# Kernel optimization log

Hardware: AMD Instinct MI355X
Metric: run time of the kernel (lower is better)

Reference implementation:

```python
import jax, jax.numpy as jnp
import numpy as np

B, L, D, K_F = 2, 1024, 768, 16  # batch, seq_len, n_embd, num_eigh**2
N_FFT = 2048


def setup_inputs() -> dict:
    key = jax.random.key(0)
    k1, k2, k3, k4 = jax.random.split(key, 4)
    x = jax.random.normal(k1, (B, L, D), dtype=jnp.float32)
    phi = jax.random.normal(k2, (L, K_F), dtype=jnp.float32) * 0.1
    M_phi_plus = jax.random.normal(k3, (K_F, D, D), dtype=jnp.float32) * (1.0 / np.sqrt(K_F * D))
    M_phi_minus = jax.random.normal(k4, (K_F, D, D), dtype=jnp.float32) * (1.0 / np.sqrt(K_F * D))
    return {"x": x, "phi": phi, "M_phi_plus": M_phi_plus, "M_phi_minus": M_phi_minus, "n": N_FFT}


def _convolve(u, v, n):
    """FFT causal convolution with K spectral filters (flash-stu `convolve`, use_approx=False).
    u: [B, L, D] inputs; v: [L, K] filters; n: FFT length (>= 2L-1 padded pow2).
    Returns U_plus, U_minus: [B, L, K, D].
    """
    b, l, d = u.shape
    sgn = jnp.where(jnp.arange(l) % 2 == 0, 1.0, -1.0).astype(u.dtype)  # alternating +/-
    # Stack the plain and sign-modulated signals: [B, L, 1, D, 2]
    U = jnp.stack([u, u * sgn[None, :, None]], axis=-1)[:, :, None, :, :]
    Uf = jnp.fft.rfft(U, n=n, axis=1)                      # [B, F, 1, D, 2] complex
    vf = jnp.fft.rfft(v, n=n, axis=0)[None, :, :, None, None]  # [1, F, K, 1, 1]
    conv = jnp.fft.irfft(vf * Uf, n=n, axis=1)[:, :l]      # [B, L, K, D, 2]
    U_plus = conv[..., 0]
    U_minus = conv[..., 1] * sgn[None, :, None, None]
    return U_plus, U_minus


def reference(x, phi, M_phi_plus, M_phi_minus, n):
    U_plus, U_minus = _convolve(x, phi, n)
    # tensordot(U, M, dims=([2,3],[0,2])): contract eigenmode k and input channel i
    spectral_plus = jnp.einsum('blki,koi->blo', U_plus, M_phi_plus)
    spectral_minus = jnp.einsum('blki,koi->blo', U_minus, M_phi_minus)
    return spectral_plus + spectral_minus
```

## Files before the change

kernel.cpp:

```cpp
#include <hip/hip_runtime.h>
#include <hip/hip_fp16.h>

typedef unsigned short u16;
typedef unsigned int   u32;
typedef _Float16 f16;
typedef __attribute__((ext_vector_type(8))) f16 f16x8;
typedef __attribute__((ext_vector_type(2))) __fp16 fp16x2;
typedef __attribute__((ext_vector_type(4))) float f32x4;

#define B_SZ  2
#define L_SEQ 1024
#define D_EMB 768
#define KF    16
#define MDIM  (B_SZ * L_SEQ)
#define KROW  (KF * D_EMB)
#define MELEM ((size_t)KF * D_EMB * D_EMB)
#define NTILE 96
#define PT_SZ 16384

__device__ __forceinline__ void gload16(const void* g, void* l) {
    __builtin_amdgcn_global_load_lds(
        (const __attribute__((address_space(1))) u32*)g,
        (__attribute__((address_space(3))) u32*)l, 16, 0, 0);
}

__global__ __launch_bounds__(256) void stu_setup(const float* __restrict__ x,
                                                 const float* __restrict__ phi,
                                                 u16* __restrict__ xT,
                                                 u16* __restrict__ Ttab) {
    __shared__ __align__(16) float xs[64][68];
    const int bid = blockIdx.x;
    const int tid = threadIdx.x;

    if (bid < 384) {
        const int s0 = (bid & 15) << 6;
        const int d0 = ((bid >> 4) % 12) << 6;
        const int b  = bid / 192;

#pragma unroll
        for (int j = 0; j < 4; ++j) {
            int c = tid + (j << 8);
            int row = c >> 4;
            int col = (c & 15) << 2;
            *(float4*)&xs[row][col] =
                *(const float4*)&x[((size_t)b * L_SEQ + s0 + row) * D_EMB + d0 + col];
        }
        __syncthreads();

        const int dl = tid >> 2;
        const int ss = (tid & 3) << 4;
        const int dg = d0 + dl;
        const int xorv = (dg & 7) << 3;

        union { u16 v[16]; uint4 q[2]; } pk;
#pragma unroll
        for (int u = 0; u < 16; ++u)
            pk.v[u] = __half_as_ushort(__float2half(xs[ss + u][dl]));

        size_t base = (size_t)b * D_EMB * L_SEQ + (size_t)dg * L_SEQ + s0;
        *(uint4*)&xT[base + ( ss      ^ xorv)] = pk.q[0];
        *(uint4*)&xT[base + ((ss + 8) ^ xorv)] = pk.q[1];
    } else {
        const int f    = bid - 384;
        const int q    = f & 15;
        const int k    = (f >> 4) & 15;
        const int sign = f >> 8;
        const int tt   = tid >> 2;
        const int ss0  = (tid & 3) << 4;

        union { u16 v[16]; uint4 q4[2]; } pk;
#pragma unroll
        for (int u = 0; u < 16; ++u) {
            int s = (q << 6) + tt - (ss0 + u);
            float v = (s >= 0 && s < L_SEQ) ? phi[s * KF + k] : 0.f;
            if (sign && (s & 1)) v = -v;
            pk.v[u] = __half_as_ushort(__float2half(v));
        }
        const int xorv = (tt & 7) << 3;
        u16* tile = Ttab + (((size_t)(sign * KF + k) * 16 + q) << 12);
        *(uint4*)&tile[(tt << 6) + ( ss0      ^ xorv)] = pk.q4[0];
        *(uint4*)&tile[(tt << 6) + ((ss0 + 8) ^ xorv)] = pk.q4[1];
    }
}

__global__ __launch_bounds__(256) void stu_conv_mcvt(
        const u16* __restrict__ xT, const u16* __restrict__ Ttab,
        u16* __restrict__ Up, u16* __restrict__ Um,
        const float* __restrict__ Mp, const float* __restrict__ Mm,
        u16* __restrict__ Hp, u16* __restrict__ Hm) {
    __shared__ __align__(16) u16 Xs[2][192 * 64];
    __shared__ __align__(16) u16 Tps[2][64 * 64];
    __shared__ __align__(16) u16 Tms[2][64 * 64];

    const int bid = blockIdx.x;
    const int tid = threadIdx.x;

    if (bid < 512) {
        const size_t n8 = MELEM / 8;
        size_t i = (size_t)bid * 256 + tid;
        const size_t stride = (size_t)512 * 256;
        for (size_t cc = i; cc < n8; cc += stride) {
            const size_t g = cc << 3;
            {
                const float4 a0 = *(const float4*)&Mp[g];
                const float4 a1 = *(const float4*)&Mp[g + 4];
                union { fp16x2 h2[4]; uint4 q; } u;
                u.h2[0] = __builtin_amdgcn_cvt_pkrtz(a0.x, a0.y);
                u.h2[1] = __builtin_amdgcn_cvt_pkrtz(a0.z, a0.w);
                u.h2[2] = __builtin_amdgcn_cvt_pkrtz(a1.x, a1.y);
                u.h2[3] = __builtin_amdgcn_cvt_pkrtz(a1.z, a1.w);
                *(uint4*)&Hp[g] = u.q;
            }
            {
                const float4 a0 = *(const float4*)&Mm[g];
                const float4 a1 = *(const float4*)&Mm[g + 4];
                union { fp16x2 h2[4]; uint4 q; } u;
                u.h2[0] = __builtin_amdgcn_cvt_pkrtz(a0.x, a0.y);
                u.h2[1] = __builtin_amdgcn_cvt_pkrtz(a0.z, a0.w);
                u.h2[2] = __builtin_amdgcn_cvt_pkrtz(a1.x, a1.y);
                u.h2[3] = __builtin_amdgcn_cvt_pkrtz(a1.z, a1.w);
                *(uint4*)&Hm[g] = u.q;
            }
        }
        return;
    }

    const int c  = bid - 512;
    const int ti = 15 - (c >> 7);
    const int t0 = ti << 6;
    const int rr = c & 127;
    const int b  = (rr >> 2) >> 4;
    const int k  = (rr >> 2) & 15;
    const int d0 = (rr & 3) * 192;

    const int lane = tid & 63;
    const int wid  = tid >> 6;
    const int wr   = wid >> 1;
    const int wc   = wid & 1;
    const int lr   = lane & 15;
    const int lk   = lane >> 4;

    f32x4 acc[2][2][6];
#pragma unroll
    for (int s = 0; s < 2; ++s)
#pragma unroll
        for (int m = 0; m < 2; ++m)
#pragma unroll
            for (int n = 0; n < 6; ++n)
                acc[s][m][n] = (f32x4){0.f, 0.f, 0.f, 0.f};

    const u16* xTb = xT + (size_t)b * D_EMB * L_SEQ + (size_t)d0 * L_SEQ;
    const u16* Tpk = Ttab + ((size_t)k * 16) * 4096;
    const u16* Tmk = Ttab + ((size_t)(KF + k) * 16) * 4096;

    auto stageX = [&](int buf, int r0) {
#pragma unroll
        for (int j = 0; j < 6; ++j) {
            int cc = tid + (j << 8);
            gload16(xTb + (size_t)(cc >> 3) * L_SEQ + r0 + ((cc & 7) << 3),
                    &Xs[buf][cc << 3]);
        }
    };
    auto stageT = [&](int buf, int q) {
        const u16* tp = Tpk + ((size_t)q << 12);
        const u16* tm = Tmk + ((size_t)q << 12);
        gload16(tp + (tid << 3),         &Tps[buf][tid << 3]);
        gload16(tp + ((tid + 256) << 3), &Tps[buf][(tid + 256) << 3]);
        gload16(tm + (tid << 3),         &Tms[buf][tid << 3]);
        gload16(tm + ((tid + 256) << 3), &Tms[buf][(tid + 256) << 3]);
    };

    stageX(0, 0);
    stageT(0, ti);
    __syncthreads();

    int cur = 0;
    for (int r0 = 0; r0 <= t0; r0 += 64) {
        if (r0 < t0) {
            stageX(cur ^ 1, r0 + 64);
            stageT(cur ^ 1, ((t0 - r0) >> 6) - 1);
        }

        const char* XsC = (const char*)&Xs[cur][0];
        const char* TpC = (const char*)&Tps[cur][0];
        const char* TmC = (const char*)&Tms[cur][0];

#pragma unroll
        for (int kk = 0; kk < 2; ++kk) {
            f16x8 bfr[6];
#pragma unroll
            for (int n = 0; n < 6; ++n) {
                const int row = wc * 96 + (n << 4) + lr;
                const int boff = ((kk << 6) + (lk << 4)) ^ ((row & 7) << 4);
                bfr[n] = *(const f16x8*)(XsC + row * 128 + boff);
            }
#pragma unroll
            for (int m = 0; m < 2; ++m) {
                const int rowt = (wr << 5) + (m << 4) + lr;
                const int aoff = ((kk << 6) + (lk << 4)) ^ ((rowt & 7) << 4);
                const f16x8 afp = *(const f16x8*)(TpC + rowt * 128 + aoff);
                const f16x8 afm = *(const f16x8*)(TmC + rowt * 128 + aoff);
#pragma unroll
                for (int n = 0; n < 6; ++n) {
                    acc[0][m][n] = __builtin_amdgcn_mfma_f32_16x16x32_f16(
                        afp, bfr[n], acc[0][m][n], 0, 0, 0);
                    acc[1][m][n] = __builtin_amdgcn_mfma_f32_16x16x32_f16(
                        afm, bfr[n], acc[1][m][n], 0, 0, 0);
                }
            }
        }
        __syncthreads();
        cur ^= 1;
    }

#pragma unroll
    for (int m = 0; m < 2; ++m) {
        const int trow = t0 + (wr << 5) + (m << 4) + (lk << 2);
#pragma unroll
        for (int n = 0; n < 6; ++n) {
            const int col = d0 + wc * 96 + (n << 4) + lr;
#pragma unroll
            for (int j = 0; j < 4; ++j) {
                size_t idx = ((size_t)(b * L_SEQ + trow + j) * KF + k) * D_EMB + col;
                Up[idx] = __half_as_ushort(__float2half(acc[0][m][n][j]));
                Um[idx] = __half_as_ushort(__float2half(acc[1][m][n][j]));
            }
        }
    }
}

__global__ __launch_bounds__(256) void stu_spectral_mfma(
        const u16* __restrict__ Up, const u16* __restrict__ Um,
        const u16* __restrict__ Mhp, const u16* __restrict__ Mhm,
        float* __restrict__ out, u16* __restrict__ P, int usePartial) {
    __shared__ __align__(16) u16 As[128 * 64];
    __shared__ __align__(16) u16 Bs[128 * 64];

    const int h   = blockIdx.x;
    const int z   = h & 7;
    const int rem = h >> 3;
    const int o0  = (rem % 6) << 7;
    const int m0  = (rem / 6) << 7;
    const int sign = z & 1;
    const int k0 = (z >> 1) << 2;

    const u16* A    = sign ? Um : Up;
    const u16* Bsrc = sign ? Mhm : Mhp;

    const int tid  = threadIdx.x;
    const int lane = tid & 63;
    const int wid  = tid >> 6;
    const int wr   = wid >> 1;
    const int wc   = wid & 1;
    const int lr   = lane & 15;
    const int lk   = lane >> 4;

    f32x4 acc[4][4];
#pragma unroll
    for (int m = 0; m < 4; ++m)
#pragma unroll
        for (int n = 0; n < 4; ++n)
            acc[m][n] = (f32x4){0.f, 0.f, 0.f, 0.f};

    for (int k = k0; k < k0 + 4; ++k) {
        const u16* Ak = A + (size_t)m0 * KROW + k * D_EMB;
        const u16* Bk = Bsrc + (size_t)k * D_EMB * D_EMB + (size_t)o0 * D_EMB;

        for (int ic = 0; ic < D_EMB; ic += 64) {
            __syncthreads();
#pragma unroll
            for (int j = 0; j < 4; ++j) {
                const int c = tid + (j << 8);
                const int row = c >> 3;
                const int off = ((c & 7) ^ (row & 7)) << 3;
                gload16(Ak + (size_t)row * KROW + ic + off, &As[c << 3]);
                gload16(Bk + (size_t)row * D_EMB + ic + off, &Bs[c << 3]);
            }
            __syncthreads();

#pragma unroll
            for (int kk = 0; kk < 2; ++kk) {
                f16x8 af[4], bf[4];
#pragma unroll
                for (int m = 0; m < 4; ++m) {
                    const int row = wr * 64 + (m << 4) + lr;
                    const int boff = (((kk << 2) + lk) ^ (row & 7)) << 4;
                    af[m] = *(const f16x8*)((const char*)&As[0] + row * 128 + boff);
                }
#pragma unroll
                for (int n = 0; n < 4; ++n) {
                    const int row = wc * 64 + (n << 4) + lr;
                    const int boff = (((kk << 2) + lk) ^ (row & 7)) << 4;
                    bf[n] = *(const f16x8*)((const char*)&Bs[0] + row * 128 + boff);
                }
#pragma unroll
                for (int m = 0; m < 4; ++m)
#pragma unroll
                    for (int n = 0; n < 4; ++n)
                        acc[m][n] = __builtin_amdgcn_mfma_f32_16x16x32_f16(
                            af[m], bf[n], acc[m][n], 0, 0, 0);
            }
        }
    }

    if (usePartial) {
        u16* Pt = P + (size_t)h * PT_SZ;
#pragma unroll
        for (int m = 0; m < 4; ++m) {
            const int rowl = wr * 64 + (m << 4) + (lk << 2);
#pragma unroll
            for (int n = 0; n < 4; ++n) {
                const int coll = wc * 64 + (n << 4) + lr;
#pragma unroll
                for (int j = 0; j < 4; ++j)
                    Pt[(rowl + j) * 128 + coll] =
                        __half_as_ushort(__float2half(acc[m][n][j]));
            }
        }
    } else {
#pragma unroll
        for (int m = 0; m < 4; ++m) {
            const int row = m0 + wr * 64 + (m << 4) + (lk << 2);
#pragma unroll
            for (int n = 0; n < 4; ++n) {
                const int col = o0 + wc * 64 + (n << 4) + lr;
#pragma unroll
                for (int j = 0; j < 4; ++j)
                    atomicAdd(&out[(size_t)(row + j) * D_EMB + col], acc[m][n][j]);
            }
        }
    }
}

__global__ __launch_bounds__(256) void stu_reduce(const u16* __restrict__ P,
                                                  float* __restrict__ out) {
    const size_t total = (size_t)MDIM * D_EMB;
    size_t idx = (size_t)blockIdx.x * 256 + threadIdx.x;
    const size_t stride = (size_t)gridDim.x * 256;
    for (; idx < total; idx += stride) {
        const int row = (int)(idx / D_EMB);
        const int col = (int)(idx % D_EMB);
        const int tile = (row >> 7) * 6 + (col >> 7);
        const u16* p = P + (size_t)tile * 8 * PT_SZ + ((row & 127) << 7) + (col & 127);
        float s = 0.f;
#pragma unroll
        for (int z = 0; z < 8; ++z)
            s += __half2float(__ushort_as_half(p[z * PT_SZ]));
        out[idx] = s;
    }
}

extern "C" void kernel_launch(void* const* d_in, const int* in_sizes, int n_in,
                              void* d_out, int out_size, void* d_ws, size_t ws_size,
                              hipStream_t stream) {
    const float* x   = (const float*)d_in[0];
    const float* phi = (const float*)d_in[1];
    const float* Mp  = (const float*)d_in[2];
    const float* Mm  = (const float*)d_in[3];
    float* out = (float*)d_out;

    const size_t S = (size_t)MDIM * KROW;
    u16* Up   = (u16*)d_ws;
    u16* Um   = Up + S;
    u16* Mhp  = Um + S;
    u16* Mhm  = Mhp + MELEM;
    u16* xT   = Mhm + MELEM;
    u16* Ttab = xT + (size_t)B_SZ * D_EMB * L_SEQ;
    u16* Part = Ttab + (size_t)2 * KF * 16 * 4096;

    const size_t elems_needed = 2 * S + 2 * MELEM + 1572864 + 2097152 + 12582912;
    const int usePartial = (ws_size >= elems_needed * sizeof(u16)) ? 1 : 0;

    if (!usePartial)
        (void)hipMemsetAsync(d_out, 0, (size_t)out_size * sizeof(float), stream);

    stu_setup<<<dim3(896), dim3(256), 0, stream>>>(x, phi, xT, Ttab);

    stu_conv_mcvt<<<dim3(2560), dim3(256), 0, stream>>>(
        xT, Ttab, Up, Um, Mp, Mm, Mhp, Mhm);

    stu_spectral_mfma<<<dim3(NTILE * 8), dim3(256), 0, stream>>>(
        Up, Um, Mhp, Mhm, out, Part, usePartial);

    if (usePartial)
        stu_reduce<<<dim3(1536), dim3(256), 0, stream>>>(Part, out);
}
```

Baseline: 171.5 us.

## Derive minus Toeplitz tile via sign-bit flip and read filter tiles directly from global

Builds only the plus-sign Toeplitz filter table and derives the sign-modulated A operand in registers by XOR-ing the fp16 sign bit of odd columns. The filter tiles are no longer staged through LDS; each wave loads its A fragments straight from global (unswizzled), which halves LDS use and allows a 3-blocks-per-CU launch bound. It also remaps block indices so each XCD works on a contiguous group of (batch, k) pairs for better L2 locality. The risks are higher global-load latency on the A fragments inside the loop, since they are no longer prefetched, and register pressure under the tighter launch bound.

```diff
diff --git a/kernel.cpp b/kernel.cpp
--- a/kernel.cpp
+++ b/kernel.cpp
@@ -61,36 +61,31 @@
         *(uint4*)&xT[base + ( ss      ^ xorv)] = pk.q[0];
         *(uint4*)&xT[base + ((ss + 8) ^ xorv)] = pk.q[1];
     } else {
-        const int f    = bid - 384;
-        const int q    = f & 15;
-        const int k    = (f >> 4) & 15;
-        const int sign = f >> 8;
-        const int tt   = tid >> 2;
-        const int ss0  = (tid & 3) << 4;
+        const int f = bid - 384;
+        const int q = f & 15;
+        const int k = f >> 4;
+        const int tt  = tid >> 2;
+        const int ss0 = (tid & 3) << 4;
 
         union { u16 v[16]; uint4 q4[2]; } pk;
 #pragma unroll
         for (int u = 0; u < 16; ++u) {
             int s = (q << 6) + tt - (ss0 + u);
             float v = (s >= 0 && s < L_SEQ) ? phi[s * KF + k] : 0.f;
-            if (sign && (s & 1)) v = -v;
             pk.v[u] = __half_as_ushort(__float2half(v));
         }
-        const int xorv = (tt & 7) << 3;
-        u16* tile = Ttab + (((size_t)(sign * KF + k) * 16 + q) << 12);
-        *(uint4*)&tile[(tt << 6) + ( ss0      ^ xorv)] = pk.q4[0];
-        *(uint4*)&tile[(tt << 6) + ((ss0 + 8) ^ xorv)] = pk.q4[1];
-    }
-}
-
-__global__ __launch_bounds__(256) void stu_conv_mcvt(
+        u16* tile = Ttab + (((size_t)k * 16 + q) << 12);
+        *(uint4*)&tile[(tt << 6) + ss0]     = pk.q4[0];
+        *(uint4*)&tile[(tt << 6) + ss0 + 8] = pk.q4[1];
+    }
+}
+
+__global__ __launch_bounds__(256, 3) void stu_conv_mcvt(
         const u16* __restrict__ xT, const u16* __restrict__ Ttab,
         u16* __restrict__ Up, u16* __restrict__ Um,
         const float* __restrict__ Mp, const float* __restrict__ Mm,
         u16* __restrict__ Hp, u16* __restrict__ Hm) {
     __shared__ __align__(16) u16 Xs[2][192 * 64];
-    __shared__ __align__(16) u16 Tps[2][64 * 64];
-    __shared__ __align__(16) u16 Tms[2][64 * 64];
 
     const int bid = blockIdx.x;
     const int tid = threadIdx.x;
@@ -125,13 +120,16 @@
         return;
     }
 
-    const int c  = bid - 512;
-    const int ti = 15 - (c >> 7);
-    const int t0 = ti << 6;
-    const int rr = c & 127;
-    const int b  = (rr >> 2) >> 4;
-    const int k  = (rr >> 2) & 15;
-    const int d0 = (rr & 3) * 192;
+    const int c    = bid - 512;
+    const int xcd  = c & 7;
+    const int w    = c >> 3;
+    const int ti   = 15 - (w >> 4);
+    const int t0   = ti << 6;
+    const int inner = w & 15;
+    const int bk   = (xcd << 2) + (inner >> 2);
+    const int b    = bk >> 4;
+    const int k    = bk & 15;
+    const int d0   = (inner & 3) * 192;
 
     const int lane = tid & 63;
     const int wid  = tid >> 6;
@@ -140,6 +138,8 @@
     const int lr   = lane & 15;
     const int lk   = lane >> 4;
 
+    const u32 xm = (lr & 1) ? 0x00008000u : 0x80000000u;
+
     f32x4 acc[2][2][6];
 #pragma unroll
     for (int s = 0; s < 2; ++s)
@@ -150,8 +150,7 @@
                 acc[s][m][n] = (f32x4){0.f, 0.f, 0.f, 0.f};
 
     const u16* xTb = xT + (size_t)b * D_EMB * L_SEQ + (size_t)d0 * L_SEQ;
-    const u16* Tpk = Ttab + ((size_t)k * 16) * 4096;
-    const u16* Tmk = Ttab + ((size_t)(KF + k) * 16) * 4096;
+    const u16* Tk  = Ttab + ((size_t)k << 16);
 
     auto stageX = [&](int buf, int r0) {
 #pragma unroll
@@ -161,30 +160,25 @@
                     &Xs[buf][cc << 3]);
         }
     };
-    auto stageT = [&](int buf, int q) {
-        const u16* tp = Tpk + ((size_t)q << 12);
-        const u16* tm = Tmk + ((size_t)q << 12);
-        gload16(tp + (tid << 3),         &Tps[buf][tid << 3]);
-        gload16(tp + ((tid + 256) << 3), &Tps[buf][(tid + 256) << 3]);
-        gload16(tm + (tid << 3),         &Tms[buf][tid << 3]);
-        gload16(tm + ((tid + 256) << 3), &Tms[buf][(tid + 256) << 3]);
-    };
 
     stageX(0, 0);
-    stageT(0, ti);
     __syncthreads();
 
     int cur = 0;
     for (int r0 = 0; r0 <= t0; r0 += 64) {
-        if (r0 < t0) {
-            stageX(cur ^ 1, r0 + 64);
-            stageT(cur ^ 1, ((t0 - r0) >> 6) - 1);
+        if (r0 < t0) stageX(cur ^ 1, r0 + 64);
+
+        const u16* TpT = Tk + ((size_t)((t0 - r0) >> 6) << 12);
+        f16x8 afp[2][2];
+#pragma unroll
+        for (int m = 0; m < 2; ++m) {
+            const int rowt = (wr << 5) + (m << 4) + lr;
+#pragma unroll
+            for (int kk = 0; kk < 2; ++kk)
+                afp[m][kk] = *(const f16x8*)&TpT[(rowt << 6) + (kk << 5) + (lk << 3)];
         }
 
         const char* XsC = (const char*)&Xs[cur][0];
-        const char* TpC = (const char*)&Tps[cur][0];
-        const char* TmC = (const char*)&Tms[cur][0];
-
 #pragma unroll
         for (int kk = 0; kk < 2; ++kk) {
             f16x8 bfr[6];
@@ -196,16 +190,18 @@
             }
 #pragma unroll
             for (int m = 0; m < 2; ++m) {
-                const int rowt = (wr << 5) + (m << 4) + lr;
-                const int aoff = ((kk << 6) + (lk << 4)) ^ ((rowt & 7) << 4);
-                const f16x8 afp = *(const f16x8*)(TpC + rowt * 128 + aoff);
-                const f16x8 afm = *(const f16x8*)(TmC + rowt * 128 + aoff);
+                const f16x8 ap = afp[m][kk];
+                union { f16x8 h; u32 wv[4]; } cv;
+                cv.h = ap;
+#pragma unroll
+                for (int qd = 0; qd < 4; ++qd) cv.wv[qd] ^= xm;
+                const f16x8 am = cv.h;
 #pragma unroll
                 for (int n = 0; n < 6; ++n) {
                     acc[0][m][n] = __builtin_amdgcn_mfma_f32_16x16x32_f16(
-                        afp, bfr[n], acc[0][m][n], 0, 0, 0);
+                        ap, bfr[n], acc[0][m][n], 0, 0, 0);
                     acc[1][m][n] = __builtin_amdgcn_mfma_f32_16x16x32_f16(
-                        afm, bfr[n], acc[1][m][n], 0, 0, 0);
+                        am, bfr[n], acc[1][m][n], 0, 0, 0);
                 }
             }
         }
@@ -366,15 +362,15 @@
     u16* Mhm  = Mhp + MELEM;
     u16* xT   = Mhm + MELEM;
     u16* Ttab = xT + (size_t)B_SZ * D_EMB * L_SEQ;
-    u16* Part = Ttab + (size_t)2 * KF * 16 * 4096;
-
-    const size_t elems_needed = 2 * S + 2 * MELEM + 1572864 + 2097152 + 12582912;
+    u16* Part = Ttab + (size_t)KF * 16 * 4096;
+
+    const size_t elems_needed = 2 * S + 2 * MELEM + 1572864 + 1048576 + 12582912;
     const int usePartial = (ws_size >= elems_needed * sizeof(u16)) ? 1 : 0;
 
     if (!usePartial)
         (void)hipMemsetAsync(d_out, 0, (size_t)out_size * sizeof(float), stream);
 
-    stu_setup<<<dim3(896), dim3(256), 0, stream>>>(x, phi, xT, Ttab);
+    stu_setup<<<dim3(640), dim3(256), 0, stream>>>(x, phi, xT, Ttab);
 
     stu_conv_mcvt<<<dim3(2560), dim3(256), 0, stream>>>(
         xT, Ttab, Up, Um, Mp, Mm, Mhp, Mhm);
```

Measured after the change: 173.6 us. Within noise of the previous version (+1.2%).
